# Kernel optimization log

Measured on AMD Instinct MI355X. Metric: run time of the kernel, lower is better.

The kernel has to match this reference:

```python
import jax, jax.numpy as jnp
import numpy as np

QUERY_DIM = 1024
KEY_DIM = 512
HIDDEN_DIM = 128
BATCH = 32
SEQ_LEN = 2048


def setup_inputs() -> dict:
    key = jax.random.key(0)
    k1, k2, k3, k4, k5 = jax.random.split(key, 5)
    query = jax.random.normal(k1, (BATCH, QUERY_DIM), dtype=jnp.float32)
    keys = jax.random.normal(k2, (BATCH, SEQ_LEN, KEY_DIM), dtype=jnp.float32)
    # nn.Linear weights, stored as (out, in) like torch; scaled ~ kaiming-uniform bound
    W1 = jax.random.normal(k3, (HIDDEN_DIM, QUERY_DIM), dtype=jnp.float32) / np.sqrt(QUERY_DIM)
    W2 = jax.random.normal(k4, (HIDDEN_DIM, KEY_DIM), dtype=jnp.float32) / np.sqrt(KEY_DIM)
    V = jax.random.normal(k5, (1, HIDDEN_DIM), dtype=jnp.float32) / np.sqrt(HIDDEN_DIM)
    return {"query": query, "keys": keys, "W1": W1, "W2": W2, "V": V}


def reference(query, keys, W1, W2, V):
    # query: [b, q], keys: [b, s, k]
    q_proj = jnp.einsum("bq,hq->bh", query, W1)          # [b, h]
    k_proj = jnp.einsum("bsk,hk->bsh", keys, W2)          # [b, s, h]
    hidden = jnp.tanh(q_proj[:, None, :] + k_proj)        # [b, s, h]
    score = jnp.einsum("bsh,oh->bs", hidden, V)           # [b, s] (o == 1)
    attention_weights = jax.nn.softmax(score, axis=1)     # [b, s]
    context = jnp.einsum("bs,bsk->bk", attention_weights, keys)  # [b, k]
    return (context, attention_weights)
```

## Files before the change

### kernel.cpp

```cpp
#include <hip/hip_runtime.h>

#define BATCH 32
#define SEQ   2048
#define KD    512
#define QD    1024
#define HD    128

#define NT 16
#define ROWS 32
#define NCHUNK 64

typedef float    f32x4 __attribute__((ext_vector_type(4)));
typedef _Float16 f16x8 __attribute__((ext_vector_type(8)));
typedef unsigned int u32;

__device__ __forceinline__ u32 pack2h(float a, float b) {
    _Float16 ha = (_Float16)a, hb = (_Float16)b;
    unsigned short ua = __builtin_bit_cast(unsigned short, ha);
    unsigned short ub = __builtin_bit_cast(unsigned short, hb);
    return (u32)ua | ((u32)ub << 16);
}

__global__ __launch_bounds__(256) void prep_kernel(
        const float* __restrict__ query, const float* __restrict__ W1,
        const float* __restrict__ W2, float* __restrict__ qp,
        char* __restrict__ w2img) {
    int blk = blockIdx.x;
    int tid = threadIdx.x;
    if (blk < 512) {
        int b = blk >> 4, hg = blk & 15;
        int wave = tid >> 6, lane = tid & 63;
        int h = hg * 8 + wave * 2 + (lane >> 5);
        int l32 = lane & 31;
        const float* q = query + (size_t)b * QD;
        const float* w = W1 + (size_t)h * QD;
        float acc = 0.f;
        #pragma unroll
        for (int i = 0; i < 8; ++i) {
            float4 qv = *(const float4*)(q + i * 128 + l32 * 4);
            float4 wv = *(const float4*)(w + i * 128 + l32 * 4);
            acc += qv.x * wv.x + qv.y * wv.y + qv.z * wv.z + qv.w * wv.w;
        }
        #pragma unroll
        for (int off = 16; off >= 1; off >>= 1) acc += __shfl_xor(acc, off);
        if (l32 == 0) qp[b * HD + h] = acc;
    } else {
        int t = blk - 512;
        #pragma unroll
        for (int rep = 0; rep < 2; ++rep) {
            int f  = tid + rep * 256;
            int hj = f >> 6;
            int ln = f & 63;
            int r  = hj * 16 + (ln & 15);
            int c  = t * 32 + (ln >> 4) * 8;
            const float* src = W2 + (size_t)r * KD + c;
            float4 v0 = *(const float4*)(src);
            float4 v1 = *(const float4*)(src + 4);
            uint4 u = make_uint4(pack2h(v0.x, v0.y), pack2h(v0.z, v0.w),
                                 pack2h(v1.x, v1.y), pack2h(v1.z, v1.w));
            *(uint4*)(w2img + ((size_t)t * 512 + f) * 16) = u;
        }
    }
}

__global__ __launch_bounds__(256, 4) void score_ctx_kernel(
        const float* __restrict__ keys, const char* __restrict__ w2img,
        const float* __restrict__ qp, const float* __restrict__ V,
        float* __restrict__ score_out, float* __restrict__ part_m,
        float* __restrict__ part_l, float* __restrict__ part_c) {
    __shared__ __align__(16) char kf16[ROWS * 1024];
    __shared__ float wpart[4][ROWS];
    __shared__ float pb[ROWS];

    const int blk  = blockIdx.x;
    const int m0   = blk * ROWS;
    const int b    = blk >> 6;
    const int tid  = threadIdx.x;
    const int wave = tid >> 6;
    const int lane = tid & 63;
    const int l15  = lane & 15;
    const int l4   = lane >> 4;

    const float4* src = (const float4*)(keys + (size_t)m0 * KD);
    #pragma unroll
    for (int i = 0; i < 16; ++i) {
        int f = i * 256 + tid;
        float4 v = src[f];
        int row = f >> 7;
        int dst = (row * 1024 + (f & 127) * 8) ^ ((row & 7) << 4);
        *(uint2*)(kf16 + dst) = make_uint2(pack2h(v.x, v.y), pack2h(v.z, v.w));
    }
    __syncthreads();

    const int hj0 = wave * 2;
    const char* bsrc = w2img + ((size_t)hj0 * 64 + lane) * 16;
    const int aswz = (l15 & 7) << 4;
    const int arow0 = l15 * 1024;
    const int arow1 = (16 + l15) * 1024;

    f32x4 acc[2][2];
    #pragma unroll
    for (int mi = 0; mi < 2; ++mi)
        #pragma unroll
        for (int hl = 0; hl < 2; ++hl)
            acc[mi][hl] = (f32x4)0.f;

    #pragma unroll
    for (int t = 0; t < NT; ++t) {
        int ac = (l4 * 16 + t * 64) ^ aswz;
        f16x8 a0 = *(const f16x8*)(kf16 + arow0 + ac);
        f16x8 a1 = *(const f16x8*)(kf16 + arow1 + ac);
        f16x8 b0 = *(const f16x8*)(bsrc + (size_t)t * 8192);
        f16x8 b1 = *(const f16x8*)(bsrc + (size_t)t * 8192 + 1024);
        acc[0][0] = __builtin_amdgcn_mfma_f32_16x16x32_f16(a0, b0, acc[0][0], 0, 0, 0);
        acc[0][1] = __builtin_amdgcn_mfma_f32_16x16x32_f16(a0, b1, acc[0][1], 0, 0, 0);
        acc[1][0] = __builtin_amdgcn_mfma_f32_16x16x32_f16(a1, b0, acc[1][0], 0, 0, 0);
        acc[1][1] = __builtin_amdgcn_mfma_f32_16x16x32_f16(a1, b1, acc[1][1], 0, 0, 0);
    }

    float qv0 = qp[b * HD + hj0 * 16 + l15];
    float qv1 = qp[b * HD + hj0 * 16 + 16 + l15];
    float vv0 = V[hj0 * 16 + l15];
    float vv1 = V[hj0 * 16 + 16 + l15];
    #pragma unroll
    for (int mi = 0; mi < 2; ++mi) {
        #pragma unroll
        for (int j = 0; j < 4; ++j) {
            float x0 = qv0 + acc[mi][0][j];
            float x1 = qv1 + acc[mi][1][j];
            float e0 = __expf(2.f * x0);
            float e1 = __expf(2.f * x1);
            float p = (1.f - 2.f * __builtin_amdgcn_rcpf(1.f + e0)) * vv0
                    + (1.f - 2.f * __builtin_amdgcn_rcpf(1.f + e1)) * vv1;
            #pragma unroll
            for (int off = 1; off < 16; off <<= 1) p += __shfl_xor(p, off);
            if (l15 == 0) wpart[wave][mi * 16 + l4 * 4 + j] = p;
        }
    }
    __syncthreads();

    int r = lane & 31;
    float prow = wpart[0][r] + wpart[1][r] + wpart[2][r] + wpart[3][r];
    float mx = prow;
    #pragma unroll
    for (int off = 1; off < 32; off <<= 1) mx = fmaxf(mx, __shfl_xor(mx, off));
    float e = __expf(prow - mx);
    float ls = e;
    #pragma unroll
    for (int off = 1; off < 32; off <<= 1) ls += __shfl_xor(ls, off);
    if (wave == 0) {
        if (lane < 32) {
            score_out[m0 + r] = prow;
            pb[r] = e;
        }
        if (lane == 0) {
            part_m[blk] = mx;
            part_l[blk] = ls;
        }
    }
    __syncthreads();

    int col = tid * 2;
    float c0 = 0.f, c1 = 0.f;
    #pragma unroll 8
    for (int s = 0; s < ROWS; ++s) {
        float w = pb[s];
        u32 kk = *(const u32*)(kf16 + ((s * 1024 + col * 2) ^ ((s & 7) << 4)));
        float k0 = (float)__builtin_bit_cast(_Float16, (unsigned short)(kk & 0xffff));
        float k1 = (float)__builtin_bit_cast(_Float16, (unsigned short)(kk >> 16));
        c0 = fmaf(w, k0, c0);
        c1 = fmaf(w, k1, c1);
    }
    *(float2*)(part_c + (size_t)blk * KD + col) = make_float2(c0, c1);
}

__global__ __launch_bounds__(256) void finalize_kernel(
        const float* __restrict__ part_m, const float* __restrict__ part_l,
        const float* __restrict__ part_c, float* __restrict__ ctx,
        float* __restrict__ wts) {
    __shared__ float eS[NCHUNK];
    int b = blockIdx.x;
    int tid = threadIdx.x;
    float M = -1e30f;
    #pragma unroll 8
    for (int i = 0; i < NCHUNK; ++i) M = fmaxf(M, part_m[b * NCHUNK + i]);
    if (tid < NCHUNK) eS[tid] = __expf(part_m[b * NCHUNK + tid] - M);
    __syncthreads();
    float L = 0.f;
    #pragma unroll 8
    for (int i = 0; i < NCHUNK; ++i) L += eS[i] * part_l[b * NCHUNK + i];
    float invL = 1.f / L;
    #pragma unroll
    for (int r = 0; r < 8; ++r) {
        int s = tid + r * 256;
        float scv = wts[b * SEQ + s];
        wts[b * SEQ + s] = __expf(scv - M) * invL;
    }
    int col = tid * 2;
    float c0 = 0.f, c1 = 0.f;
    #pragma unroll 8
    for (int i = 0; i < NCHUNK; ++i) {
        float w = eS[i];
        float2 pc = *(const float2*)(part_c + (size_t)(b * NCHUNK + i) * KD + col);
        c0 = fmaf(w, pc.x, c0);
        c1 = fmaf(w, pc.y, c1);
    }
    ctx[b * KD + col]     = c0 * invL;
    ctx[b * KD + col + 1] = c1 * invL;
}

extern "C" void kernel_launch(void* const* d_in, const int* in_sizes, int n_in,
                              void* d_out, int out_size, void* d_ws, size_t ws_size,
                              hipStream_t stream) {
    const float* query = (const float*)d_in[0];
    const float* keys  = (const float*)d_in[1];
    const float* W1    = (const float*)d_in[2];
    const float* W2    = (const float*)d_in[3];
    const float* V     = (const float*)d_in[4];

    float* ctx = (float*)d_out;
    float* wts = (float*)d_out + BATCH * KD;

    char* wsb     = (char*)d_ws;
    float* qp     = (float*)wsb;
    char*  w2img  = wsb + 16 * 1024;
    float* part_m = (float*)(wsb + 144 * 1024);
    float* part_l = (float*)(wsb + 152 * 1024);
    float* part_c = (float*)(wsb + 160 * 1024);

    prep_kernel<<<528, 256, 0, stream>>>(query, W1, W2, qp, w2img);
    score_ctx_kernel<<<BATCH * NCHUNK, 256, 0, stream>>>(
        keys, w2img, qp, V, wts, part_m, part_l, part_c);
    finalize_kernel<<<BATCH, 256, 0, stream>>>(part_m, part_l, part_c, ctx, wts);
}
```

Baseline: 54.11 us.

## Load keys directly into LDS as fp32 and halve rows per block

```diff
diff --git a/kernel.cpp b/kernel.cpp
--- a/kernel.cpp
+++ b/kernel.cpp
@@ -7,8 +7,8 @@
 #define HD    128
 
 #define NT 16
-#define ROWS 32
-#define NCHUNK 64
+#define ROWS 16
+#define NCHUNK 128
 
 typedef float    f32x4 __attribute__((ext_vector_type(4)));
 typedef _Float16 f16x8 __attribute__((ext_vector_type(8)));
@@ -19,6 +19,18 @@
     unsigned short ua = __builtin_bit_cast(unsigned short, ha);
     unsigned short ub = __builtin_bit_cast(unsigned short, hb);
     return (u32)ua | ((u32)ub << 16);
+}
+
+__device__ __forceinline__ f16x8 cvtA4(const f32x4& r0, const f32x4& r1) {
+    uint4 u = make_uint4(pack2h(r0[0], r0[1]), pack2h(r0[2], r0[3]),
+                         pack2h(r1[0], r1[1]), pack2h(r1[2], r1[3]));
+    return __builtin_bit_cast(f16x8, u);
+}
+
+__device__ __forceinline__ void gload_lds16(const void* g, void* l) {
+    __builtin_amdgcn_global_load_lds(
+        (const __attribute__((address_space(1))) unsigned int*)g,
+        (__attribute__((address_space(3))) unsigned int*)l, 16, 0, 0);
 }
 
 __global__ __launch_bounds__(256) void prep_kernel(
@@ -68,54 +80,48 @@
         const float* __restrict__ qp, const float* __restrict__ V,
         float* __restrict__ score_out, float* __restrict__ part_m,
         float* __restrict__ part_l, float* __restrict__ part_c) {
-    __shared__ __align__(16) char kf16[ROWS * 1024];
+    __shared__ __align__(16) char kf[ROWS * 2048];
     __shared__ float wpart[4][ROWS];
     __shared__ float pb[ROWS];
 
     const int blk  = blockIdx.x;
     const int m0   = blk * ROWS;
-    const int b    = blk >> 6;
+    const int b    = blk >> 7;
     const int tid  = threadIdx.x;
     const int wave = tid >> 6;
     const int lane = tid & 63;
     const int l15  = lane & 15;
     const int l4   = lane >> 4;
 
-    const float4* src = (const float4*)(keys + (size_t)m0 * KD);
-    #pragma unroll
-    for (int i = 0; i < 16; ++i) {
-        int f = i * 256 + tid;
-        float4 v = src[f];
-        int row = f >> 7;
-        int dst = (row * 1024 + (f & 127) * 8) ^ ((row & 7) << 4);
-        *(uint2*)(kf16 + dst) = make_uint2(pack2h(v.x, v.y), pack2h(v.z, v.w));
+    {
+        const char* kb = (const char*)(keys + (size_t)m0 * KD);
+        #pragma unroll
+        for (int j = 0; j < 8; ++j) {
+            int row  = wave * 4 + (j >> 1);
+            int slot = (j & 1) * 64 + lane;
+            int gg   = slot ^ (row & 7);
+            gload_lds16(kb + (size_t)row * 2048 + gg * 16,
+                        kf + wave * 8192 + j * 1024 + lane * 16);
+        }
     }
     __syncthreads();
 
     const int hj0 = wave * 2;
     const char* bsrc = w2img + ((size_t)hj0 * 64 + lane) * 16;
-    const int aswz = (l15 & 7) << 4;
-    const int arow0 = l15 * 1024;
-    const int arow1 = (16 + l15) * 1024;
-
-    f32x4 acc[2][2];
-    #pragma unroll
-    for (int mi = 0; mi < 2; ++mi)
-        #pragma unroll
-        for (int hl = 0; hl < 2; ++hl)
-            acc[mi][hl] = (f32x4)0.f;
-
+    const char* arow = kf + l15 * 2048;
+    const int r7 = l15 & 7;
+
+    f32x4 acc0 = (f32x4)0.f, acc1 = (f32x4)0.f;
     #pragma unroll
     for (int t = 0; t < NT; ++t) {
-        int ac = (l4 * 16 + t * 64) ^ aswz;
-        f16x8 a0 = *(const f16x8*)(kf16 + arow0 + ac);
-        f16x8 a1 = *(const f16x8*)(kf16 + arow1 + ac);
+        int g = l4 * 2 + t * 8;
+        f32x4 a0 = *(const f32x4*)(arow + ((g ^ r7) * 16));
+        f32x4 a1 = *(const f32x4*)(arow + (((g + 1) ^ r7) * 16));
+        f16x8 af = cvtA4(a0, a1);
         f16x8 b0 = *(const f16x8*)(bsrc + (size_t)t * 8192);
         f16x8 b1 = *(const f16x8*)(bsrc + (size_t)t * 8192 + 1024);
-        acc[0][0] = __builtin_amdgcn_mfma_f32_16x16x32_f16(a0, b0, acc[0][0], 0, 0, 0);
-        acc[0][1] = __builtin_amdgcn_mfma_f32_16x16x32_f16(a0, b1, acc[0][1], 0, 0, 0);
-        acc[1][0] = __builtin_amdgcn_mfma_f32_16x16x32_f16(a1, b0, acc[1][0], 0, 0, 0);
-        acc[1][1] = __builtin_amdgcn_mfma_f32_16x16x32_f16(a1, b1, acc[1][1], 0, 0, 0);
+        acc0 = __builtin_amdgcn_mfma_f32_16x16x32_f16(af, b0, acc0, 0, 0, 0);
+        acc1 = __builtin_amdgcn_mfma_f32_16x16x32_f16(af, b1, acc1, 0, 0, 0);
     }
 
     float qv0 = qp[b * HD + hj0 * 16 + l15];
@@ -123,53 +129,48 @@
     float vv0 = V[hj0 * 16 + l15];
     float vv1 = V[hj0 * 16 + 16 + l15];
     #pragma unroll
-    for (int mi = 0; mi < 2; ++mi) {
-        #pragma unroll
-        for (int j = 0; j < 4; ++j) {
-            float x0 = qv0 + acc[mi][0][j];
-            float x1 = qv1 + acc[mi][1][j];
-            float e0 = __expf(2.f * x0);
-            float e1 = __expf(2.f * x1);
-            float p = (1.f - 2.f * __builtin_amdgcn_rcpf(1.f + e0)) * vv0
-                    + (1.f - 2.f * __builtin_amdgcn_rcpf(1.f + e1)) * vv1;
-            #pragma unroll
-            for (int off = 1; off < 16; off <<= 1) p += __shfl_xor(p, off);
-            if (l15 == 0) wpart[wave][mi * 16 + l4 * 4 + j] = p;
-        }
-    }
-    __syncthreads();
-
-    int r = lane & 31;
+    for (int j = 0; j < 4; ++j) {
+        float x0 = qv0 + acc0[j];
+        float x1 = qv1 + acc1[j];
+        float e0 = __expf(2.f * x0);
+        float e1 = __expf(2.f * x1);
+        float p = (1.f - 2.f * __builtin_amdgcn_rcpf(1.f + e0)) * vv0
+                + (1.f - 2.f * __builtin_amdgcn_rcpf(1.f + e1)) * vv1;
+        #pragma unroll
+        for (int off = 1; off < 16; off <<= 1) p += __shfl_xor(p, off);
+        if (l15 == 0) wpart[wave][l4 * 4 + j] = p;
+    }
+    __syncthreads();
+
+    int r = lane & 15;
     float prow = wpart[0][r] + wpart[1][r] + wpart[2][r] + wpart[3][r];
     float mx = prow;
     #pragma unroll
-    for (int off = 1; off < 32; off <<= 1) mx = fmaxf(mx, __shfl_xor(mx, off));
+    for (int off = 1; off < 16; off <<= 1) mx = fmaxf(mx, __shfl_xor(mx, off));
     float e = __expf(prow - mx);
     float ls = e;
     #pragma unroll
-    for (int off = 1; off < 32; off <<= 1) ls += __shfl_xor(ls, off);
-    if (wave == 0) {
-        if (lane < 32) {
-            score_out[m0 + r] = prow;
-            pb[r] = e;
-        }
-        if (lane == 0) {
-            part_m[blk] = mx;
-            part_l[blk] = ls;
-        }
-    }
-    __syncthreads();
-
-    int col = tid * 2;
+    for (int off = 1; off < 16; off <<= 1) ls += __shfl_xor(ls, off);
+    if (wave == 0 && lane < 16) {
+        score_out[m0 + r] = prow;
+        pb[r] = e;
+    }
+    if (tid == 0) {
+        part_m[blk] = mx;
+        part_l[blk] = ls;
+    }
+    __syncthreads();
+
+    int col  = tid * 2;
+    int gsl  = tid >> 1;
+    int off8 = (tid & 1) * 8;
     float c0 = 0.f, c1 = 0.f;
-    #pragma unroll 8
+    #pragma unroll 4
     for (int s = 0; s < ROWS; ++s) {
-        float w = pb[s];
-        u32 kk = *(const u32*)(kf16 + ((s * 1024 + col * 2) ^ ((s & 7) << 4)));
-        float k0 = (float)__builtin_bit_cast(_Float16, (unsigned short)(kk & 0xffff));
-        float k1 = (float)__builtin_bit_cast(_Float16, (unsigned short)(kk >> 16));
-        c0 = fmaf(w, k0, c0);
-        c1 = fmaf(w, k1, c1);
+        const char* p = kf + s * 2048 + ((gsl ^ (s & 7)) * 16) + off8;
+        float2 kv = *(const float2*)p;
+        c0 = fmaf(pb[s], kv.x, c0);
+        c1 = fmaf(pb[s], kv.y, c1);
     }
     *(float2*)(part_c + (size_t)blk * KD + col) = make_float2(c0, c1);
 }
@@ -225,8 +226,8 @@
     float* qp     = (float*)wsb;
     char*  w2img  = wsb + 16 * 1024;
     float* part_m = (float*)(wsb + 144 * 1024);
-    float* part_l = (float*)(wsb + 152 * 1024);
-    float* part_c = (float*)(wsb + 160 * 1024);
+    float* part_l = (float*)(wsb + 160 * 1024);
+    float* part_c = (float*)(wsb + 176 * 1024);
 
     prep_kernel<<<528, 256, 0, stream>>>(query, W1, W2, qp, w2img);
     score_ctx_kernel<<<BATCH * NCHUNK, 256, 0, stream>>>(
```

New measurement: 70.99 us. 31.2% more time.
